# Kernel tuning notes

Measured on AMD Instinct MI355X. Metric: run time of the kernel, lower is better.

## Reference

```python
import jax, jax.numpy as jnp
import numpy as np

N_NODES = 50000
N_EDGES = 800000
N_GRAPHS = 512
D_NODE = 64
D_EDGE = 32
Z_DIM = 2 * D_NODE + D_EDGE  # 160


def setup_inputs() -> dict:
    key = jax.random.key(0)
    ks = jax.random.split(key, 12)
    inp = {
        'x': jax.random.normal(ks[0], (N_NODES, D_NODE), dtype=jnp.float32),
        'edge_index': jax.random.randint(ks[1], (2, N_EDGES), 0, N_NODES, dtype=jnp.int64),
        'edge_attr': jax.random.uniform(ks[2], (N_EDGES, D_EDGE), dtype=jnp.float32),
        'batch': jnp.sort(jax.random.randint(ks[3], (N_NODES,), 0, N_GRAPHS, dtype=jnp.int64)),
        'Wf1': jax.random.normal(ks[4], (Z_DIM, D_NODE), dtype=jnp.float32) * 0.05,
        'bf1': jnp.zeros((D_NODE,), dtype=jnp.float32),
        'Ws1': jax.random.normal(ks[5], (Z_DIM, D_NODE), dtype=jnp.float32) * 0.05,
        'bs1': jnp.zeros((D_NODE,), dtype=jnp.float32),
        'Wf2': jax.random.normal(ks[6], (Z_DIM, D_NODE), dtype=jnp.float32) * 0.05,
        'bf2': jnp.zeros((D_NODE,), dtype=jnp.float32),
        'Ws2': jax.random.normal(ks[7], (Z_DIM, D_NODE), dtype=jnp.float32) * 0.05,
        'bs2': jnp.zeros((D_NODE,), dtype=jnp.float32),
        'W_out': jax.random.normal(ks[8], (D_NODE, 1), dtype=jnp.float32) * 0.05,
        'b_out': jnp.zeros((1,), dtype=jnp.float32),
    }
    return inp


def _cgconv(x, edge_index, edge_attr, Wf, bf, Ws, bs):
    # PyG CGConv: out_i = x_i + sum_{j in N(i)} sigmoid(lin_f(z_ij)) * softplus(lin_s(z_ij))
    # with z_ij = [x_i, x_j, e_ij]; source_to_target flow: j=edge_index[0], i=edge_index[1]
    src, dst = edge_index[0], edge_index[1]
    z = jnp.concatenate([x[dst], x[src], edge_attr], axis=-1)  # [E, 2d+dim]
    msg = jax.nn.sigmoid(z @ Wf + bf) * jax.nn.softplus(z @ Ws + bs)  # [E, d]
    aggr = jax.ops.segment_sum(msg, dst, num_segments=x.shape[0])
    return x + aggr


def reference(x, edge_index, edge_attr, batch, Wf1, bf1, Ws1, bs1, Wf2, bf2, Ws2, bs2, W_out, b_out):
    h = _cgconv(x, edge_index, edge_attr, Wf1, bf1, Ws1, bs1)
    h = _cgconv(h, edge_index, edge_attr, Wf2, bf2, Ws2, bs2)
    pooled = jax.ops.segment_sum(h, batch, num_segments=N_GRAPHS)  # global_add_pool [G, d]
    out = pooled @ W_out + b_out  # [G, 1]
    return out
```

## Files before the change

kernel.cpp:

```cpp
#include <hip/hip_runtime.h>
#include <math.h>

#define N_NODES 50000
#define N_EDGES 800000
#define N_GRAPHS 512
#define D 64
#define DE 32
#define NB_SCAN 196
#define NSTR 136
#define NB_SCAT 3125
#define NB_NT 1563


typedef __attribute__((ext_vector_type(8))) short short8;
typedef __attribute__((ext_vector_type(4))) float floatx4;
union Frag { short8 s; unsigned u[4]; };
union U4   { uint4 v; unsigned u[4]; };

__device__ inline unsigned pk_bf16(float lo, float hi) {
    unsigned a = __float_as_uint(lo);
    unsigned b = __float_as_uint(hi);
    a = (a + 0x7FFFu + ((a >> 16) & 1u)) >> 16;
    b = (b + 0x7FFFu + ((b >> 16) & 1u)) >> 16;
    return a | (b << 16);
}
__device__ inline unsigned short bf16_1(float v) {
    unsigned a = __float_as_uint(v);
    return (unsigned short)((a + 0x7FFFu + ((a >> 16) & 1u)) >> 16);
}
__device__ inline float upk(unsigned u16) { return __uint_as_float(u16 << 16); }

__global__ __launch_bounds__(256) void hist_kernel(
    const int* __restrict__ ei, int* __restrict__ deg)
{
    int e = blockIdx.x * 256 + threadIdx.x;
    atomicAdd(&deg[ei[N_EDGES + e]], 1);
}

__global__ __launch_bounds__(256) void scan1(
    const int* __restrict__ deg, int* __restrict__ off, int* __restrict__ tsum)
{
    __shared__ int s[256];
    int i = blockIdx.x * 256 + threadIdx.x;
    s[threadIdx.x] = (i < N_NODES) ? deg[i] : 0;
    __syncthreads();
    if (threadIdx.x == 0) {
        int run = 0;
        for (int k = 0; k < 256; ++k) { int t = s[k]; s[k] = run; run += t; }
        tsum[blockIdx.x] = run;
    }
    __syncthreads();
    if (i < N_NODES) off[i] = s[threadIdx.x];
}

__global__ __launch_bounds__(256) void scan2(int* __restrict__ tsum)
{
    __shared__ int s[256];
    int i = threadIdx.x;
    s[i] = (i < NB_SCAN) ? tsum[i] : 0;
    __syncthreads();
    if (i == 0) {
        int run = 0;
        for (int k = 0; k < NB_SCAN; ++k) { int t = s[k]; s[k] = run; run += t; }
    }
    __syncthreads();
    if (i < NB_SCAN) tsum[i] = s[i];
}

__global__ __launch_bounds__(256) void scan3(
    int* __restrict__ off, const int* __restrict__ tsum)
{
    int i = blockIdx.x * 256 + threadIdx.x;
    if (i < N_NODES) off[i] += tsum[blockIdx.x];
    if (i == N_NODES) off[i] = N_EDGES;
}

__global__ __launch_bounds__(256) void pack_W(
    const float* __restrict__ Wf1, const float* __restrict__ Ws1,
    const float* __restrict__ Wf2, const float* __restrict__ Ws2,
    uint4* __restrict__ WpkNT, uint4* __restrict__ WpkE)
{
    const int layer = blockIdx.y;
    const float* Wf = layer ? Wf2 : Wf1;
    const float* Ws = layer ? Ws2 : Ws1;
    const int i = blockIdx.x * 256 + threadIdx.x;
    if (i < 1024) {
        const int p    = i >> 9;
        const int cbi  = (i >> 6) & 7;
        const int l    = i & 63;
        const int n16  = l & 15, quad = l >> 4, kc = quad * 8;
        const int col  = cbi * 16 + n16;
        const int j    = col >> 1;
        const float* Wsel = (col & 1) ? Ws : Wf;
        const int rbase = p * 64;
        U4 b0, b1;
#pragma unroll
        for (int pp = 0; pp < 4; ++pp) {
            b0.u[pp] = pk_bf16(Wsel[(rbase + kc + 2 * pp) * 64 + j],
                               Wsel[(rbase + kc + 2 * pp + 1) * 64 + j]);
            b1.u[pp] = pk_bf16(Wsel[(rbase + 32 + kc + 2 * pp) * 64 + j],
                               Wsel[(rbase + 32 + kc + 2 * pp + 1) * 64 + j]);
        }
        uint4* o = WpkNT + ((size_t)layer * 1024 + i) * 2;
        o[0] = b0.v; o[1] = b1.v;
    } else if (i < 1280) {
        const int k  = i - 1024;
        const int jb = k >> 6;
        const int l  = k & 63;
        const int n16 = l & 15, quad = l >> 4, c0 = quad * 8;
        const int j = jb * 16 + n16;
        U4 bf_, bs_;
#pragma unroll
        for (int pp = 0; pp < 4; ++pp) {
            bf_.u[pp] = pk_bf16(Wf[(128 + c0 + 2 * pp) * 64 + j],
                                Wf[(128 + c0 + 2 * pp + 1) * 64 + j]);
            bs_.u[pp] = pk_bf16(Ws[(128 + c0 + 2 * pp) * 64 + j],
                                Ws[(128 + c0 + 2 * pp + 1) * 64 + j]);
        }
        uint4* o = WpkE + ((size_t)layer * 256 + k) * 2;
        o[0] = bf_.v; o[1] = bs_.v;
    }
}

__global__ __launch_bounds__(256) void fused_scatter_nt(
    const int* __restrict__ ei, const int* __restrict__ off,
    int* __restrict__ cnt, const float* __restrict__ ea,
    unsigned short* __restrict__ eaS, int2* __restrict__ sd_sorted,
    const float* __restrict__ H,
    const float* __restrict__ bf, const float* __restrict__ bs,
    const uint4* __restrict__ Wpk,
    unsigned short* __restrict__ Tdst, unsigned short* __restrict__ Tsrc,
    float* __restrict__ hinit)
{
    __shared__ unsigned short lt[4][16 * NSTR];

    if (blockIdx.x < NB_SCAT) {
        int e = blockIdx.x * 256 + threadIdx.x;
        int s = ei[e];
        int d = ei[N_EDGES + e];
        int r = atomicAdd(&cnt[d], 1);
        int pos = off[d] + r;
        sd_sorted[pos] = make_int2(s, d);

        const float4* src4 = (const float4*)(ea + (size_t)e * 32);
        uint4* dst16 = (uint4*)(eaS + (size_t)pos * 32);
#pragma unroll
        for (int q = 0; q < 2; ++q) {
            float4 v0 = src4[4 * q + 0];
            float4 v1 = src4[4 * q + 1];
            float4 v2 = src4[4 * q + 2];
            float4 v3 = src4[4 * q + 3];
            uint4 o0;
            o0.x = pk_bf16(v0.x, v0.y); o0.y = pk_bf16(v0.z, v0.w);
            o0.z = pk_bf16(v1.x, v1.y); o0.w = pk_bf16(v1.z, v1.w);
            uint4 o1;
            o1.x = pk_bf16(v2.x, v2.y); o1.y = pk_bf16(v2.z, v2.w);
            o1.z = pk_bf16(v3.x, v3.y); o1.w = pk_bf16(v3.z, v3.w);
            dst16[2 * q + 0] = o0;
            dst16[2 * q + 1] = o1;
        }
        return;
    }

    const int lane = threadIdx.x & 63;
    const int wid  = threadIdx.x >> 6;
    const int n16  = lane & 15;
    const int quad = lane >> 4;
    const int kc   = quad * 8;
    unsigned short* L = lt[wid];

    const int gid = (blockIdx.x - NB_SCAT) * 4 + wid;
    const int NW  = (N_NODES / 16) * 2;
    if (gid >= NW) return;
    const int ntile = gid >> 1;
    const int part  = gid & 1;
    unsigned short* Tout = part ? Tsrc : Tdst;

    const float* hrow = H + (size_t)(ntile * 16 + n16) * D;
    float4 q0 = *(const float4*)(hrow + kc);
    float4 q1 = *(const float4*)(hrow + kc + 4);
    float4 q2 = *(const float4*)(hrow + 32 + kc);
    float4 q3 = *(const float4*)(hrow + 32 + kc + 4);
    Frag a0, a1;
    a0.u[0] = pk_bf16(q0.x, q0.y); a0.u[1] = pk_bf16(q0.z, q0.w);
    a0.u[2] = pk_bf16(q1.x, q1.y); a0.u[3] = pk_bf16(q1.z, q1.w);
    a1.u[0] = pk_bf16(q2.x, q2.y); a1.u[1] = pk_bf16(q2.z, q2.w);
    a1.u[2] = pk_bf16(q3.x, q3.y); a1.u[3] = pk_bf16(q3.z, q3.w);

    if (part == 0) {
        float4* hp = (float4*)(hinit + (size_t)(ntile * 16 + n16) * D);
        hp[quad * 2]     = q0;
        hp[quad * 2 + 1] = q1;
        hp[8 + quad * 2] = q2;
        hp[9 + quad * 2] = q3;
    }

#pragma unroll
    for (int cbi = 0; cbi < 8; ++cbi) {
        const int col   = cbi * 16 + n16;
        const int sflag = col & 1;
        const int j     = col >> 1;

        Frag b0, b1;
        {
            const uint4* bp = Wpk + ((size_t)(part * 512 + cbi * 64 + lane)) * 2;
            *(uint4*)&b0 = bp[0];
            *(uint4*)&b1 = bp[1];
        }
        float bias = 0.0f;
        if (part == 0) bias = sflag ? bs[j] : bf[j];

        floatx4 acc = {bias, bias, bias, bias};
        acc = __builtin_amdgcn_mfma_f32_16x16x32_bf16(a0.s, b0.s, acc, 0, 0, 0);
        acc = __builtin_amdgcn_mfma_f32_16x16x32_bf16(a1.s, b1.s, acc, 0, 0, 0);

#pragma unroll
        for (int r = 0; r < 4; ++r)
            L[(quad * 4 + r) * NSTR + col] = bf16_1(acc[r]);
    }

#pragma unroll
    for (int it = 0; it < 4; ++it) {
        const int node_l = it * 4 + quad;
        const int c8     = n16 * 8;
        uint4 v = *(const uint4*)(L + node_l * NSTR + c8);
        *(uint4*)(Tout + (size_t)(ntile * 16 + node_l) * 128 + c8) = v;
    }
}

__global__ __launch_bounds__(256) void node_transform_mfma(
    const float* __restrict__ H,
    const float* __restrict__ bf,
    const float* __restrict__ bs,
    const uint4* __restrict__ Wpk,
    unsigned short* __restrict__ Tdst,
    unsigned short* __restrict__ Tsrc,
    float* __restrict__ hinit)
{
    __shared__ unsigned short lt[4][16 * NSTR];
    const int lane = threadIdx.x & 63;
    const int wid  = threadIdx.x >> 6;
    const int n16  = lane & 15;
    const int quad = lane >> 4;
    const int kc   = quad * 8;
    unsigned short* L = lt[wid];

    const int gid = blockIdx.x * 4 + wid;
    const int NW  = (N_NODES / 16) * 2;
    if (gid >= NW) return;
    const int ntile = gid >> 1;
    const int part  = gid & 1;
    unsigned short* Tout = part ? Tsrc : Tdst;

    const float* hrow = H + (size_t)(ntile * 16 + n16) * D;
    float4 q0 = *(const float4*)(hrow + kc);
    float4 q1 = *(const float4*)(hrow + kc + 4);
    float4 q2 = *(const float4*)(hrow + 32 + kc);
    float4 q3 = *(const float4*)(hrow + 32 + kc + 4);
    Frag a0, a1;
    a0.u[0] = pk_bf16(q0.x, q0.y); a0.u[1] = pk_bf16(q0.z, q0.w);
    a0.u[2] = pk_bf16(q1.x, q1.y); a0.u[3] = pk_bf16(q1.z, q1.w);
    a1.u[0] = pk_bf16(q2.x, q2.y); a1.u[1] = pk_bf16(q2.z, q2.w);
    a1.u[2] = pk_bf16(q3.x, q3.y); a1.u[3] = pk_bf16(q3.z, q3.w);

    if (part == 0) {
        float4* hp = (float4*)(hinit + (size_t)(ntile * 16 + n16) * D);
        hp[quad * 2]     = q0;
        hp[quad * 2 + 1] = q1;
        hp[8 + quad * 2] = q2;
        hp[9 + quad * 2] = q3;
    }

#pragma unroll
    for (int cbi = 0; cbi < 8; ++cbi) {
        const int col   = cbi * 16 + n16;
        const int sflag = col & 1;
        const int j     = col >> 1;

        Frag b0, b1;
        {
            const uint4* bp = Wpk + ((size_t)(part * 512 + cbi * 64 + lane)) * 2;
            *(uint4*)&b0 = bp[0];
            *(uint4*)&b1 = bp[1];
        }
        float bias = 0.0f;
        if (part == 0) bias = sflag ? bs[j] : bf[j];

        floatx4 acc = {bias, bias, bias, bias};
        acc = __builtin_amdgcn_mfma_f32_16x16x32_bf16(a0.s, b0.s, acc, 0, 0, 0);
        acc = __builtin_amdgcn_mfma_f32_16x16x32_bf16(a1.s, b1.s, acc, 0, 0, 0);

#pragma unroll
        for (int r = 0; r < 4; ++r)
            L[(quad * 4 + r) * NSTR + col] = bf16_1(acc[r]);
    }

#pragma unroll
    for (int it = 0; it < 4; ++it) {
        const int node_l = it * 4 + quad;
        const int c8     = n16 * 8;
        uint4 v = *(const uint4*)(L + node_l * NSTR + c8);
        *(uint4*)(Tout + (size_t)(ntile * 16 + node_l) * 128 + c8) = v;
    }
}

__global__ __launch_bounds__(256) void edge_message_mfma(
    const unsigned short* __restrict__ Tdst,
    const unsigned short* __restrict__ Tsrc,
    const unsigned short* __restrict__ eaS,
    const int2* __restrict__ sd_sorted,
    const uint4* __restrict__ WpkE,
    float* __restrict__ hout)
{
    const int lane = threadIdx.x & 63;
    const int wid  = threadIdx.x >> 6;
    const int n16  = lane & 15;
    const int quad = lane >> 4;
    const int c0   = quad * 8;

    Frag bfr[4], bsr[4];
#pragma unroll
    for (int jb = 0; jb < 4; ++jb) {
        *(uint4*)&bfr[jb] = WpkE[((size_t)(jb * 64 + lane)) * 2 + 0];
        *(uint4*)&bsr[jb] = WpkE[((size_t)(jb * 64 + lane)) * 2 + 1];
    }

    const int nwg = gridDim.x;
    const int xcd = blockIdx.x & 7;
    const int idx = blockIdx.x >> 3;
    const int q   = nwg >> 3, rr = nwg & 7;
    const int sb  = (xcd < rr ? xcd * (q + 1) : rr * (q + 1) + (xcd - rr) * q) + idx;
    const int w   = sb * 4 + wid;
    const int base = w * 64;

    const floatx4 zero = {0.0f, 0.0f, 0.0f, 0.0f};

    const unsigned short* aptr =
        eaS + (size_t)(base + (n16 >> 2) * 16 + (n16 & 3)) * 32 + c0;
    Frag af0, af1, af2, af3;
    af0.s = *(const short8*)(aptr);
    af1.s = *(const short8*)(aptr + 128);
    af2.s = *(const short8*)(aptr + 256);
    af3.s = *(const short8*)(aptr + 384);

    const int4* sdp4 = (const int4*)(sd_sorted + base + quad * 16);
    int4 sdq[8];
#pragma unroll
    for (int i = 0; i < 8; ++i) sdq[i] = sdp4[i];

#define SV(e) ((((e) & 1) != 0) ? sdq[(e) >> 1].z : sdq[(e) >> 1].x)
#define DV(e) ((((e) & 1) != 0) ? sdq[(e) >> 1].w : sdq[(e) >> 1].y)

    int cur_d = -1;
    unsigned dr0 = 0, dr1 = 0, dr2 = 0, dr3 = 0;
    float acc0 = 0.f, acc1 = 0.f, acc2 = 0.f, acc3 = 0.f;

#pragma unroll
    for (int tt = 0; tt < 4; ++tt) {
        unsigned s0[4], s1[4], s2[4], s3[4];
#pragma unroll
        for (int r = 0; r < 4; ++r) {
            const unsigned* srow =
                (const unsigned*)(Tsrc + (size_t)SV(4 * tt + r) * 128);
            s0[r] = srow[n16];
            s1[r] = srow[16 + n16];
            s2[r] = srow[32 + n16];
            s3[r] = srow[48 + n16];
        }

        const Frag& af = (tt == 0) ? af0 : (tt == 1) ? af1 : (tt == 2) ? af2 : af3;
        floatx4 accf[4], accs[4];
#pragma unroll
        for (int jb = 0; jb < 4; ++jb) {
            accf[jb] = __builtin_amdgcn_mfma_f32_16x16x32_bf16(af.s, bfr[jb].s, zero, 0, 0, 0);
            accs[jb] = __builtin_amdgcn_mfma_f32_16x16x32_bf16(af.s, bsr[jb].s, zero, 0, 0, 0);
        }

#pragma unroll
        for (int r = 0; r < 4; ++r) {
            const int dv = DV(4 * tt + r);
            if (dv != cur_d) {
                if (cur_d >= 0) {
                    float* hp = hout + (size_t)cur_d * D + n16;
                    atomicAdd(hp +  0, acc0);
                    atomicAdd(hp + 16, acc1);
                    atomicAdd(hp + 32, acc2);
                    atomicAdd(hp + 48, acc3);
                }
                cur_d = dv;
                const unsigned* drow = (const unsigned*)(Tdst + (size_t)dv * 128);
                dr0 = drow[n16];
                dr1 = drow[16 + n16];
                dr2 = drow[32 + n16];
                dr3 = drow[48 + n16];
                acc0 = acc1 = acc2 = acc3 = 0.f;
            }
#pragma unroll
            for (int jb = 0; jb < 4; ++jb) {
                unsigned d2 = (jb == 0) ? dr0 : (jb == 1) ? dr1 : (jb == 2) ? dr2 : dr3;
                unsigned sv = (jb == 0) ? s0[r] : (jb == 1) ? s1[r] : (jb == 2) ? s2[r] : s3[r];
                float vf = accf[jb][r] + upk(d2 & 0xFFFFu) + upk(sv & 0xFFFFu);
                float vs = accs[jb][r] + upk(d2 >> 16) + upk(sv >> 16);
                float sig = __builtin_amdgcn_rcpf(1.0f + __expf(-vf));
                float spl = fmaxf(vs, 0.0f) + __logf(1.0f + __expf(-fabsf(vs)));
                float msg = sig * spl;
                if      (jb == 0) acc0 += msg;
                else if (jb == 1) acc1 += msg;
                else if (jb == 2) acc2 += msg;
                else              acc3 += msg;
            }
        }
    }
#undef SV
#undef DV
    {
        float* hp = hout + (size_t)cur_d * D + n16;
        atomicAdd(hp +  0, acc0);
        atomicAdd(hp + 16, acc1);
        atomicAdd(hp + 32, acc2);
        atomicAdd(hp + 48, acc3);
    }
}

__global__ __launch_bounds__(256) void pool_kernel(
    const float* __restrict__ h,
    const int* __restrict__ batch,
    float* __restrict__ pooled)
{
    const int lane = threadIdx.x & 63;
    const int wid  = threadIdx.x >> 6;
    const int w = blockIdx.x * 4 + wid;
    const int n0 = w * 16;
    if (n0 >= N_NODES) return;
    const int nend = (n0 + 16 < N_NODES) ? (n0 + 16) : N_NODES;

    int cur = batch[n0];
    float acc = 0.0f;
    for (int n = n0; n < nend; ++n) {
        int b = batch[n];
        float v = h[(size_t)n * D + lane];
        if (b != cur) {
            atomicAdd(&pooled[(size_t)cur * D + lane], acc);
            cur = b; acc = v;
        } else {
            acc += v;
        }
    }
    atomicAdd(&pooled[(size_t)cur * D + lane], acc);
}

__global__ __launch_bounds__(256) void out_kernel(
    const float* __restrict__ pooled,
    const float* __restrict__ Wout,
    const float* __restrict__ bout,
    float* __restrict__ out)
{
    const int g = blockIdx.x * blockDim.x + threadIdx.x;
    if (g >= N_GRAPHS) return;
    float acc = bout[0];
#pragma unroll
    for (int j = 0; j < D; ++j) acc = fmaf(pooled[(size_t)g * D + j], Wout[j], acc);
    out[g] = acc;
}

extern "C" void kernel_launch(void* const* d_in, const int* in_sizes, int n_in,
                              void* d_out, int out_size, void* d_ws, size_t ws_size,
                              hipStream_t stream) {
    const float* x     = (const float*)d_in[0];
    const int*   ei    = (const int*)  d_in[1];
    const float* ea    = (const float*)d_in[2];
    const int*   batch = (const int*)  d_in[3];
    const float* Wf1   = (const float*)d_in[4];
    const float* bf1   = (const float*)d_in[5];
    const float* Ws1   = (const float*)d_in[6];
    const float* bs1   = (const float*)d_in[7];
    const float* Wf2   = (const float*)d_in[8];
    const float* bf2   = (const float*)d_in[9];
    const float* Ws2   = (const float*)d_in[10];
    const float* bs2   = (const float*)d_in[11];
    const float* Wout  = (const float*)d_in[12];
    const float* bout  = (const float*)d_in[13];
    float* out = (float*)d_out;

    char* base = (char*)d_ws;
    size_t o = 0;
    unsigned short* Tdst = (unsigned short*)(base + o); o += (size_t)N_NODES * 128 * 2;
    unsigned short* Tsrc = (unsigned short*)(base + o); o += (size_t)N_NODES * 128 * 2;
    unsigned short* eaS  = (unsigned short*)(base + o); o += (size_t)N_EDGES * 32 * 2;
    float* h1     = (float*)(base + o); o += (size_t)N_NODES * D * 4;
    float* h2     = (float*)(base + o); o += (size_t)N_NODES * D * 4;
    float* pooled = (float*)(base + o); o += (size_t)N_GRAPHS * D * 4;
    int* deg  = (int*)(base + o); o += (size_t)N_NODES * 4;
    int* off  = (int*)(base + o); o += (size_t)(N_NODES + 1) * 4;
    int* tsum = (int*)(base + o); o += 256 * 4;
    int2* sd_sorted = (int2*)(base + o); o += (size_t)N_EDGES * 8;
    uint4* WpkNT = (uint4*)(base + o); o += (size_t)2 * 1024 * 2 * 16;
    uint4* WpkE  = (uint4*)(base + o); o += (size_t)2 * 256 * 2 * 16;

    pack_W<<<dim3(5, 2), 256, 0, stream>>>(Wf1, Ws1, Wf2, Ws2, WpkNT, WpkE);

    hipMemsetAsync(deg, 0, (size_t)N_NODES * 4, stream);
    hist_kernel<<<N_EDGES / 256, 256, 0, stream>>>(ei, deg);
    scan1<<<NB_SCAN, 256, 0, stream>>>(deg, off, tsum);
    scan2<<<1, 256, 0, stream>>>(tsum);
    scan3<<<NB_SCAN, 256, 0, stream>>>(off, tsum);
    hipMemsetAsync(deg, 0, (size_t)N_NODES * 4, stream);

    fused_scatter_nt<<<NB_SCAT + NB_NT, 256, 0, stream>>>(
        ei, off, deg, ea, eaS, sd_sorted,
        x, bf1, bs1, WpkNT, Tdst, Tsrc, h1);

    edge_message_mfma<<<3125, 256, 0, stream>>>(Tdst, Tsrc, eaS, sd_sorted,
                                                WpkE, h1);

    node_transform_mfma<<<1563, 256, 0, stream>>>(h1, bf2, bs2, WpkNT + 2048, Tdst, Tsrc, h2);
    edge_message_mfma<<<3125, 256, 0, stream>>>(Tdst, Tsrc, eaS, sd_sorted,
                                                WpkE + 512, h2);

    hipMemsetAsync(pooled, 0, (size_t)N_GRAPHS * D * 4, stream);
    pool_kernel<<<782, 256, 0, stream>>>(h2, batch, pooled);
    out_kernel<<<2, 256, 0, stream>>>(pooled, Wout, bout, out);
}
```

Measured before the change: 440.7 us.

## Reuse histogram atomic ranks, interleave scatter/NT blocks, double-buffer edge gathers

The histogram kernel now records each edge's atomic rank, so the scatter no longer needs a second pass of atomics or the memset that reset the counters. Scatter blocks and node-transform blocks are interleaved 2:1 in the fused launch rather than placed in two contiguous ranges, so both kinds of work run at the same time. In the edge-message kernel, source-row gathers and edge-attribute fragments are software-prefetched one tile ahead to hide load latency, at the cost of more registers. The rank array is aliased onto h2, which is not written until later.

```diff
diff --git a/kernel.cpp b/kernel.cpp
--- a/kernel.cpp
+++ b/kernel.cpp
@@ -10,6 +10,7 @@
 #define NSTR 136
 #define NB_SCAT 3125
 #define NB_NT 1563
+#define NB_FUSED 4689
 
 
 typedef __attribute__((ext_vector_type(8))) short short8;
@@ -31,10 +32,10 @@
 __device__ inline float upk(unsigned u16) { return __uint_as_float(u16 << 16); }
 
 __global__ __launch_bounds__(256) void hist_kernel(
-    const int* __restrict__ ei, int* __restrict__ deg)
+    const int* __restrict__ ei, int* __restrict__ deg, int* __restrict__ rank)
 {
     int e = blockIdx.x * 256 + threadIdx.x;
-    atomicAdd(&deg[ei[N_EDGES + e]], 1);
+    rank[e] = atomicAdd(&deg[ei[N_EDGES + e]], 1);
 }
 
 __global__ __launch_bounds__(256) void scan1(
@@ -124,7 +125,7 @@
 
 __global__ __launch_bounds__(256) void fused_scatter_nt(
     const int* __restrict__ ei, const int* __restrict__ off,
-    int* __restrict__ cnt, const float* __restrict__ ea,
+    const int* __restrict__ rank, const float* __restrict__ ea,
     unsigned short* __restrict__ eaS, int2* __restrict__ sd_sorted,
     const float* __restrict__ H,
     const float* __restrict__ bf, const float* __restrict__ bs,
@@ -133,13 +134,15 @@
     float* __restrict__ hinit)
 {
     __shared__ unsigned short lt[4][16 * NSTR];
-
-    if (blockIdx.x < NB_SCAT) {
-        int e = blockIdx.x * 256 + threadIdx.x;
+    const int k = blockIdx.x;
+
+    if ((k % 3) != 2) {
+        const int sid = k - (k / 3);
+        if (sid >= NB_SCAT) return;
+        int e = sid * 256 + threadIdx.x;
         int s = ei[e];
         int d = ei[N_EDGES + e];
-        int r = atomicAdd(&cnt[d], 1);
-        int pos = off[d] + r;
+        int pos = off[d] + rank[e];
         sd_sorted[pos] = make_int2(s, d);
 
         const float4* src4 = (const float4*)(ea + (size_t)e * 32);
@@ -169,7 +172,7 @@
     const int kc   = quad * 8;
     unsigned short* L = lt[wid];
 
-    const int gid = (blockIdx.x - NB_SCAT) * 4 + wid;
+    const int gid = (k / 3) * 4 + wid;
     const int NW  = (N_NODES / 16) * 2;
     if (gid >= NW) return;
     const int ntile = gid >> 1;
@@ -335,21 +338,28 @@
 
     const floatx4 zero = {0.0f, 0.0f, 0.0f, 0.0f};
 
+    const int4* sdp4 = (const int4*)(sd_sorted + base + quad * 16);
+    int4 sdq[8];
+#pragma unroll
+    for (int i = 0; i < 8; ++i) sdq[i] = sdp4[i];
+
+#define SV(e) ((((e) & 1) != 0) ? sdq[(e) >> 1].z : sdq[(e) >> 1].x)
+#define DV(e) ((((e) & 1) != 0) ? sdq[(e) >> 1].w : sdq[(e) >> 1].y)
+
     const unsigned short* aptr =
         eaS + (size_t)(base + (n16 >> 2) * 16 + (n16 & 3)) * 32 + c0;
-    Frag af0, af1, af2, af3;
-    af0.s = *(const short8*)(aptr);
-    af1.s = *(const short8*)(aptr + 128);
-    af2.s = *(const short8*)(aptr + 256);
-    af3.s = *(const short8*)(aptr + 384);
-
-    const int4* sdp4 = (const int4*)(sd_sorted + base + quad * 16);
-    int4 sdq[8];
-#pragma unroll
-    for (int i = 0; i < 8; ++i) sdq[i] = sdp4[i];
-
-#define SV(e) ((((e) & 1) != 0) ? sdq[(e) >> 1].z : sdq[(e) >> 1].x)
-#define DV(e) ((((e) & 1) != 0) ? sdq[(e) >> 1].w : sdq[(e) >> 1].y)
+    Frag af;
+    af.s = *(const short8*)aptr;
+
+    unsigned sbuf[2][4][4];
+#pragma unroll
+    for (int r = 0; r < 4; ++r) {
+        const unsigned* srow = (const unsigned*)(Tsrc + (size_t)SV(r) * 128);
+        sbuf[0][r][0] = srow[n16];
+        sbuf[0][r][1] = srow[16 + n16];
+        sbuf[0][r][2] = srow[32 + n16];
+        sbuf[0][r][3] = srow[48 + n16];
+    }
 
     int cur_d = -1;
     unsigned dr0 = 0, dr1 = 0, dr2 = 0, dr3 = 0;
@@ -357,24 +367,26 @@
 
 #pragma unroll
     for (int tt = 0; tt < 4; ++tt) {
-        unsigned s0[4], s1[4], s2[4], s3[4];
-#pragma unroll
-        for (int r = 0; r < 4; ++r) {
-            const unsigned* srow =
-                (const unsigned*)(Tsrc + (size_t)SV(4 * tt + r) * 128);
-            s0[r] = srow[n16];
-            s1[r] = srow[16 + n16];
-            s2[r] = srow[32 + n16];
-            s3[r] = srow[48 + n16];
-        }
-
-        const Frag& af = (tt == 0) ? af0 : (tt == 1) ? af1 : (tt == 2) ? af2 : af3;
+        const int cb = tt & 1, nb = cb ^ 1;
+        if (tt < 3) {
+#pragma unroll
+            for (int r = 0; r < 4; ++r) {
+                const unsigned* srow =
+                    (const unsigned*)(Tsrc + (size_t)SV(4 * (tt + 1) + r) * 128);
+                sbuf[nb][r][0] = srow[n16];
+                sbuf[nb][r][1] = srow[16 + n16];
+                sbuf[nb][r][2] = srow[32 + n16];
+                sbuf[nb][r][3] = srow[48 + n16];
+            }
+        }
+
         floatx4 accf[4], accs[4];
 #pragma unroll
         for (int jb = 0; jb < 4; ++jb) {
             accf[jb] = __builtin_amdgcn_mfma_f32_16x16x32_bf16(af.s, bfr[jb].s, zero, 0, 0, 0);
             accs[jb] = __builtin_amdgcn_mfma_f32_16x16x32_bf16(af.s, bsr[jb].s, zero, 0, 0, 0);
         }
+        if (tt < 3) af.s = *(const short8*)(aptr + (tt + 1) * 128);
 
 #pragma unroll
         for (int r = 0; r < 4; ++r) {
@@ -398,7 +410,7 @@
 #pragma unroll
             for (int jb = 0; jb < 4; ++jb) {
                 unsigned d2 = (jb == 0) ? dr0 : (jb == 1) ? dr1 : (jb == 2) ? dr2 : dr3;
-                unsigned sv = (jb == 0) ? s0[r] : (jb == 1) ? s1[r] : (jb == 2) ? s2[r] : s3[r];
+                unsigned sv = sbuf[cb][r][jb];
                 float vf = accf[jb][r] + upk(d2 & 0xFFFFu) + upk(sv & 0xFFFFu);
                 float vs = accs[jb][r] + upk(d2 >> 16) + upk(sv >> 16);
                 float sig = __builtin_amdgcn_rcpf(1.0f + __expf(-vf));
@@ -496,18 +508,18 @@
     int2* sd_sorted = (int2*)(base + o); o += (size_t)N_EDGES * 8;
     uint4* WpkNT = (uint4*)(base + o); o += (size_t)2 * 1024 * 2 * 16;
     uint4* WpkE  = (uint4*)(base + o); o += (size_t)2 * 256 * 2 * 16;
+    int* rank = (int*)h2;
 
     pack_W<<<dim3(5, 2), 256, 0, stream>>>(Wf1, Ws1, Wf2, Ws2, WpkNT, WpkE);
 
     hipMemsetAsync(deg, 0, (size_t)N_NODES * 4, stream);
-    hist_kernel<<<N_EDGES / 256, 256, 0, stream>>>(ei, deg);
+    hist_kernel<<<N_EDGES / 256, 256, 0, stream>>>(ei, deg, rank);
     scan1<<<NB_SCAN, 256, 0, stream>>>(deg, off, tsum);
     scan2<<<1, 256, 0, stream>>>(tsum);
     scan3<<<NB_SCAN, 256, 0, stream>>>(off, tsum);
-    hipMemsetAsync(deg, 0, (size_t)N_NODES * 4, stream);
-
-    fused_scatter_nt<<<NB_SCAT + NB_NT, 256, 0, stream>>>(
-        ei, off, deg, ea, eaS, sd_sorted,
+
+    fused_scatter_nt<<<NB_FUSED, 256, 0, stream>>>(
+        ei, off, rank, ea, eaS, sd_sorted,
         x, bf1, bs1, WpkNT, Tdst, Tsrc, h1);
 
     edge_message_mfma<<<3125, 256, 0, stream>>>(Tdst, Tsrc, eaS, sd_sorted,
```

Result: no change. 446.5 us (+1.3%).
